# Performance work log

Measured on AMD Instinct MI355X. Metric: run time of the kernel, lower is better.

## Reference

```python
import jax, jax.numpy as jnp
import numpy as np

B, C, N, T = 32, 32, 300, 64      # batch, residual/conv channels, nodes, seq_len
DIM, K, SKIP, GD = 40, 20, 64, 2  # node_dim, top-k (subgraph_size), skip_channels, gcn_depth
TANH_A, PROP_A = 3.0, 0.05
KSET = (2, 3, 6, 7)
TOUT = T - (KSET[-1] - 1)          # 58: time length after dilated inception (dilation=1)


def conv2d(x, w, b):
    y = jax.lax.conv_general_dilated(x, w, (1, 1), 'VALID', dimension_numbers=('NCHW', 'OIHW', 'NCHW'))
    return y + b[None, :, None, None]


def setup_inputs() -> dict:
    key = jax.random.key(0)
    ks = iter(jax.random.split(key, 48))
    def nrm(shape, s=1.0):
        return jax.random.normal(next(ks), shape, jnp.float32) * s
    inp = {
        'x': nrm((B, C, N, T)),
        'x_skip': nrm((B, SKIP, N, 1)),
        'idx': jnp.arange(N, dtype=jnp.int32),
        'emb1': nrm((N, DIM), 0.1), 'emb2': nrm((N, DIM), 0.1),
        'lin1_w': nrm((DIM, DIM), 0.15), 'lin1_b': jnp.zeros((DIM,), jnp.float32),
        'lin2_w': nrm((DIM, DIM), 0.15), 'lin2_b': jnp.zeros((DIM,), jnp.float32),
        'skip_w': nrm((SKIP, C, 1, TOUT), 0.05), 'skip_b': jnp.zeros((SKIP,), jnp.float32),
        'mp1_w': nrm((C, (GD + 1) * C, 1, 1), 0.1), 'mp1_b': jnp.zeros((C,), jnp.float32),
        'mp2_w': nrm((C, (GD + 1) * C, 1, 1), 0.1), 'mp2_b': jnp.zeros((C,), jnp.float32),
        'ln_w': jnp.ones((C, N, TOUT), jnp.float32), 'ln_b': jnp.zeros((C, N, TOUT), jnp.float32),
    }
    for k in KSET:
        inp[f'fw{k}'] = nrm((C // 4, C, 1, k), 0.1); inp[f'fb{k}'] = jnp.zeros((C // 4,), jnp.float32)
        inp[f'gw{k}'] = nrm((C // 4, C, 1, k), 0.1); inp[f'gb{k}'] = jnp.zeros((C // 4,), jnp.float32)
    return inp


def _forward(x, x_skip, idx, emb1, emb2, lin1_w, lin1_b, lin2_w, lin2_b,
             fws, gws, skip_w, skip_b, mp1_w, mp1_b, mp2_w, mp2_b, ln_w, ln_b):
    # --- GraphConstructor: learned sparse adjacency via tanh/relu/top-k/scatter ---
    n1 = jnp.tanh(TANH_A * (emb1[idx] @ lin1_w.T + lin1_b))
    n2 = jnp.tanh(TANH_A * (emb2[idx] @ lin2_w.T + lin2_b))
    a = n1 @ n2.T - n2 @ n1.T
    A = jax.nn.relu(jnp.tanh(TANH_A * a))
    _, cols = jax.lax.top_k(A, K)                               # [N, K] per-row top-k indices
    mask = jnp.zeros_like(A).at[jnp.arange(N)[:, None], cols].set(1.0)
    A = A * mask
    # --- DilatedInception filter/gate (Conv2d kernel (1,k), crop to shortest) ---
    Xf = jnp.tanh(jnp.concatenate([conv2d(x, w, b)[..., -TOUT:] for w, b in fws], axis=1))
    Xg = jax.nn.sigmoid(jnp.concatenate([conv2d(x, w, b)[..., -TOUT:] for w, b in gws], axis=1))
    X = Xf * Xg                                                 # dropout is identity (training=False)
    X_skip_out = conv2d(X, skip_w, skip_b) + x_skip             # [B, SKIP, N, 1]
    # --- MixProp graph diffusion over A and A^T ---
    def mixprop(Xin, Adj, w, b):
        Ah = Adj + jnp.eye(N, dtype=Adj.dtype)
        Ah = Ah / Ah.sum(1)[:, None]                            # row-normalize
        H, hops = Xin, [Xin]
        for _ in range(GD):
            H = PROP_A * Xin + (1.0 - PROP_A) * jnp.einsum('bcwt,vw->bcvt', H, Ah)
            hops.append(H)
        return conv2d(jnp.concatenate(hops, axis=1), w, b)      # 1x1 conv: (GD+1)*C -> C
    X = mixprop(X, A, mp1_w, mp1_b) + mixprop(X, A.T, mp2_w, mp2_b)
    X = X + x[..., -TOUT:]
    # --- LayerNorm over (C, N, TOUT) with node-indexed affine ---
    mu = X.mean(axis=(1, 2, 3), keepdims=True)
    var = ((X - mu) ** 2).mean(axis=(1, 2, 3), keepdims=True)
    Xn = (X - mu) * jax.lax.rsqrt(var + 1e-5)
    X = Xn * ln_w[:, idx, :][None] + ln_b[:, idx, :][None]
    return X, X_skip_out


def reference(x, x_skip, idx, emb1, emb2, lin1_w, lin1_b, lin2_w, lin2_b,
              fw2, fb2, fw3, fb3, fw6, fb6, fw7, fb7,
              gw2, gb2, gw3, gb3, gw6, gb6, gw7, gb7,
              skip_w, skip_b, mp1_w, mp1_b, mp2_w, mp2_b, ln_w, ln_b):
    fws = [(fw2, fb2), (fw3, fb3), (fw6, fb6), (fw7, fb7)]
    gws = [(gw2, gb2), (gw3, gb3), (gw6, gb6), (gw7, gb7)]
    return _forward(x, x_skip, idx, emb1, emb2, lin1_w, lin1_b, lin2_w, lin2_b,
                    fws, gws, skip_w, skip_b, mp1_w, mp1_b, mp2_w, mp2_b, ln_w, ln_b)
```

## Files before the change

### kernel.cpp

```cpp
#include <hip/hip_runtime.h>
#include <hip/hip_bf16.h>
#include <math.h>

typedef __hip_bfloat16 bf16;
typedef __attribute__((ext_vector_type(8))) short bf16x8;
typedef __attribute__((ext_vector_type(4))) float f32x4;

#define NB 32
#define NC 32
#define NNODE 300
#define NT 64
#define NDIM 40
#define KTOP 20
#define NSKIP 64
#define NTOUT 58
#define SLAB 17400
#define BSLAB 556800
#define XEL 17817600
#define PSLAB 2048
#define BPSLAB 614400
#define XPEL 19660800

__device__ __forceinline__ float b2f(bf16 v){ return __bfloat162float(v); }
__device__ __forceinline__ bf16 f2b(float v){ return __float2bfloat16(v); }
__device__ __forceinline__ float fsig(float x){ return 1.0f/(1.0f + __expf(-x)); }
__device__ __forceinline__ float ftanh(float x){ return 2.0f*fsig(2.0f*x) - 1.0f; }

__device__ __forceinline__ unsigned short bbits(float v){
  bf16 h = f2b(v); unsigned short s; __builtin_memcpy(&s, &h, 2); return s;
}

__device__ __forceinline__ uint4 pack8(const float f[8]){
  uint4 d;
  d.x = (unsigned)bbits(f[0]) | ((unsigned)bbits(f[1]) << 16);
  d.y = (unsigned)bbits(f[2]) | ((unsigned)bbits(f[3]) << 16);
  d.z = (unsigned)bbits(f[4]) | ((unsigned)bbits(f[5]) << 16);
  d.w = (unsigned)bbits(f[6]) | ((unsigned)bbits(f[7]) << 16);
  return d;
}

__device__ __forceinline__ void bv_swz(int bid, int& b, int& v){
  int xcd = bid & 7, i = bid >> 3;
  int nb = xcd*1200 + i;
  b = nb / NNODE; v = nb - b*NNODE;
}

__global__ void k_nodes(const float* __restrict__ emb1, const float* __restrict__ emb2,
                        const float* __restrict__ l1w, const float* __restrict__ l1b,
                        const float* __restrict__ l2w, const float* __restrict__ l2b,
                        const int* __restrict__ idxp,
                        float* __restrict__ n1, float* __restrict__ n2){
  int i = blockIdx.x; int d = threadIdx.x;
  if (d >= NDIM) return;
  int r = idxp[i];
  float a1 = l1b[d], a2 = l2b[d];
  for (int k=0;k<NDIM;++k){
    a1 = fmaf(emb1[r*NDIM+k], l1w[d*NDIM+k], a1);
    a2 = fmaf(emb2[r*NDIM+k], l2w[d*NDIM+k], a2);
  }
  n1[i*NDIM+d] = tanhf(3.0f*a1);
  n2[i*NDIM+d] = tanhf(3.0f*a2);
}

__global__ void __launch_bounds__(64) k_adjrow(const float* __restrict__ n1,
                                               const float* __restrict__ n2,
                                               float* __restrict__ Am){
  int i = blockIdx.x; int lane = threadIdx.x;
  __shared__ float rowo[NNODE];
  __shared__ float rowv[NNODE];
  __shared__ int   sel[NNODE];
  for (int j=lane;j<NNODE;j+=64){
    float a = 0.f;
    #pragma unroll
    for (int k=0;k<NDIM;++k){
      float a1 = n1[i*NDIM+k], a2 = n2[i*NDIM+k];
      a = fmaf(a1, n2[j*NDIM+k], a);
      a = fmaf(-a2, n1[j*NDIM+k], a);
    }
    float v = tanhf(3.0f*a);
    v = v > 0.f ? v : 0.f;
    rowo[j]=v; rowv[j]=v; sel[j]=0;
  }
  __syncthreads();
  for (int it=0; it<KTOP; ++it){
    float best = -1.f; int bi = 0x7fffffff;
    for (int j=lane;j<NNODE;j+=64){
      float v = rowv[j];
      if (v > best){ best=v; bi=j; }
    }
    #pragma unroll
    for (int off=32; off; off>>=1){
      float ov = __shfl_xor(best, off);
      int   oi = __shfl_xor(bi, off);
      if (ov > best || (ov == best && oi < bi)){ best=ov; bi=oi; }
    }
    if (lane==0){ sel[bi]=1; rowv[bi]=-2.f; }
    __syncthreads();
  }
  for (int j=lane;j<NNODE;j+=64)
    Am[i*NNODE+j] = sel[j] ? rowo[j] : 0.f;
}

__global__ void __launch_bounds__(64) k_norm(const float* __restrict__ Am, float* __restrict__ Ah){
  int r = blockIdx.x;
  int side = r >= 304; int v = side ? r - 304 : r;
  float* dst = Ah + (size_t)(side ? 304*304 : 0) + v*304;
  int lane = threadIdx.x;
  if (v >= NNODE){
    for (int w=lane; w<304; w+=64) dst[w] = 0.f;
    return;
  }
  float s = 0.f;
  for (int w=lane; w<NNODE; w+=64)
    s += side ? Am[w*NNODE + v] : Am[v*NNODE + w];
  #pragma unroll
  for (int off=32; off; off>>=1) s += __shfl_xor(s, off);
  float inv = 1.0f/(s + 1.0f);
  for (int w=lane; w<304; w+=64){
    float a = (w < NNODE) ? (side ? Am[w*NNODE + v] : Am[v*NNODE + w]) : 0.f;
    if (w == v) a += 1.0f;
    dst[w] = a*inv;
  }
}

__global__ void k_mpk(const float* __restrict__ Ah, bf16* __restrict__ Mpk){
  int id = blockIdx.x*blockDim.x + threadIdx.x;
  if (id >= 4*320*320) return;
  int pm = id / (320*320);
  int rem = id % (320*320);
  int v = rem / 320, w = rem % 320;
  int s = pm >> 1, m = pm & 1;
  float val = 0.f;
  if (v < 304 && w < 304){
    const float* A = Ah + (size_t)s*304*304;
    float a = A[v*304 + w];
    if (m == 0){
      val = 0.95f*a + (v==w ? 0.05f : 0.f);
    } else {
      float d = 0.f;
      for (int u=0; u<304; ++u) d = fmaf(A[v*304 + u], A[u*304 + w], d);
      val = 0.9025f*d + 0.0475f*a + (v==w ? 0.05f : 0.f);
    }
  }
  int vt16 = v >> 4, lv = v & 15, ks = w >> 5, g = (w >> 3) & 3, j = w & 7;
  int lane = g*16 + lv;
  Mpk[(((size_t)(pm*20 + vt16)*10 + ks)*64 + lane)*8 + j] = f2b(val);
}

__global__ void k_wpack2(const float* __restrict__ fw2,const float* __restrict__ fw3,
                         const float* __restrict__ fw6,const float* __restrict__ fw7,
                         const float* __restrict__ gw2,const float* __restrict__ gw3,
                         const float* __restrict__ gw6,const float* __restrict__ gw7,
                         const float* __restrict__ fb2,const float* __restrict__ fb3,
                         const float* __restrict__ fb6,const float* __restrict__ fb7,
                         const float* __restrict__ gb2,const float* __restrict__ gb3,
                         const float* __restrict__ gb6,const float* __restrict__ gb7,
                         bf16* __restrict__ wfA, float* __restrict__ biasPk){
  int T = blockIdx.x*blockDim.x + threadIdx.x;
  if (T < 14336){
    int j = T & 7;
    int l = (T >> 3) & 63;
    int q = T >> 9;
    int d = q % 7, mt = q / 7;
    int m = mt*16 + (l & 15);
    int ic = (l >> 4)*8 + j;
    int c = m >> 1, path = m & 1;
    int cls = c >> 3, o = c & 7;
    int kk = (cls==0) ? 2 : (cls==1) ? 3 : (cls==2) ? 6 : 7;
    int tp = d - (7 - kk);
    float val = 0.f;
    if (tp >= 0){
      const float* w = (path==0)
        ? (cls==0?fw2:cls==1?fw3:cls==2?fw6:fw7)
        : (cls==0?gw2:cls==1?gw3:cls==2?gw6:gw7);
      val = w[(o*NC + ic)*kk + tp];
    }
    wfA[T] = f2b(val);
  } else if (T < 14336 + 32){
    int c = T - 14336;
    int cls = c >> 3, o = c & 7;
    const float* fb = cls==0?fb2:cls==1?fb3:cls==2?fb6:fb7;
    const float* gb = cls==0?gb2:cls==1?gb3:cls==2?gb6:gb7;
    biasPk[c*2]   = fb[o];
    biasPk[c*2+1] = gb[o];
  }
}

__global__ void k_wprepM(const float* __restrict__ m1w, const float* __restrict__ m2w,
                         const float* __restrict__ m1b, const float* __restrict__ m2b,
                         bf16* __restrict__ pkB0, bf16* __restrict__ pkB1,
                         float* __restrict__ biasSum){
  int id = blockIdx.x*blockDim.x + threadIdx.x;
  if (id < 3072){
    int j = id & 7, l = (id >> 3) & 63, q = id >> 9;
    int ks = q % 3, nt = q / 3;
    int k = (l >> 4)*8 + j;
    int c = nt*16 + (l & 15);
    float val;
    if      (ks == 0) val = m1w[c*96 + k] + m2w[c*96 + k];
    else if (ks == 1) val = m1w[c*96 + 32 + k];
    else              val = m1w[c*96 + 64 + k];
    pkB0[id] = f2b(val);
  } else if (id < 5120){
    int id2 = id - 3072;
    int j = id2 & 7, l = (id2 >> 3) & 63, q = id2 >> 9;
    int ks = q & 1, nt = q >> 1;
    int k = (l >> 4)*8 + j;
    int c = nt*16 + (l & 15);
    pkB1[id2] = f2b(ks==0 ? m2w[c*96 + 32 + k] : m2w[c*96 + 64 + k]);
  } else if (id < 5152){
    int c = id - 5120;
    biasSum[c] = m1b[c] + m2b[c];
  }
}

__global__ void k_wTb(const float* __restrict__ sw, bf16* __restrict__ wTb){
  int id = blockIdx.x*blockDim.x + threadIdx.x;
  if (id >= 131072) return;
  int j = id & 7, l = (id >> 3) & 63, q = id >> 9;
  int ks = q & 63, nt = q >> 6;
  int k = ks*32 + (l >> 4)*8 + j;
  int t = k >> 5, c = k & 31;
  int sc = nt*16 + (l & 15);
  float val = (t < NTOUT) ? sw[sc*1856 + c*NTOUT + t] : 0.f;
  wTb[id] = f2b(val);
}

__global__ void __launch_bounds__(256) k_incepM(const float* __restrict__ x,
    const bf16* __restrict__ wfA, const float* __restrict__ biasPk,
    bf16* __restrict__ Xp){
  __shared__ unsigned short xcm[72*32];
  int b, n; bv_swz(blockIdx.x, b, n);
  int bn = b*NNODE + n;
  int tid = threadIdx.x;
  {
    int c = tid >> 3, tq = tid & 7, t0 = tq*8;
    const float* src = x + ((size_t)(b*NC + c)*NNODE + n)*NT + t0;
    float4 v0 = *reinterpret_cast<const float4*>(src);
    float4 v1 = *reinterpret_cast<const float4*>(src + 4);
    float f[8] = {v0.x,v0.y,v0.z,v0.w,v1.x,v1.y,v1.z,v1.w};
    int gl = c >> 3, cl = c & 7;
    #pragma unroll
    for (int i=0;i<8;++i){
      int t = t0 + i;
      int pg = gl ^ ((t >> 3) & 3);
      xcm[t*32 + pg*8 + cl] = bbits(f[i]);
    }
    int zt = 64 + (tid >> 5), zic = tid & 31;
    int zpg = (zic >> 3) ^ ((zt >> 3) & 3);
    xcm[zt*32 + zpg*8 + (zic & 7)] = 0;
  }
  __syncthreads();
  int lane = tid & 63;
  int mt = __builtin_amdgcn_readfirstlane(tid >> 6);
  bf16x8 wA[7];
  #pragma unroll
  for (int d=0; d<7; ++d)
    wA[d] = *reinterpret_cast<const bf16x8*>(wfA + (size_t)((mt*7 + d)*64 + lane)*8);
  int g = lane >> 4, col = lane & 15;
  int c0 = mt*8 + 2*g;
  float4 bias2 = *reinterpret_cast<const float4*>(biasPk + c0*2);
  #pragma unroll
  for (int nt=0; nt<4; ++nt){
    int t = col + nt*16;
    f32x4 acc = {0.f, 0.f, 0.f, 0.f};
    #pragma unroll
    for (int d=0; d<7; ++d){
      int tr = t + d;
      int pg = g ^ ((tr >> 3) & 3);
      bf16x8 bfr = *reinterpret_cast<const bf16x8*>(&xcm[tr*32 + pg*8]);
      acc = __builtin_amdgcn_mfma_f32_16x16x32_bf16(wA[d], bfr, acc, 0, 0, 0);
    }
    bool act = t < NTOUT;
    float X0 = act ? (ftanh(acc[0] + bias2.x) * fsig(acc[1] + bias2.y)) : 0.f;
    float X1 = act ? (ftanh(acc[2] + bias2.z) * fsig(acc[3] + bias2.w)) : 0.f;
    unsigned pv = (unsigned)bbits(X0) | ((unsigned)bbits(X1) << 16);
    *reinterpret_cast<unsigned*>(Xp + (size_t)bn*PSLAB + t*32 + c0) = pv;
  }
}

__global__ void __launch_bounds__(256) k_xt(const bf16* __restrict__ Xp, bf16* __restrict__ XpT2){
  __shared__ unsigned short tile[64*66];
  int bid = blockIdx.x;
  int b = bid / 160, r = bid - b*160;
  int wt = r / 32, ctt2 = r - wt*32;
  int w0 = wt*64, ct0 = ctt2*64;
  int tid = threadIdx.x;
  #pragma unroll
  for (int p=0; p<2; ++p){
    int w_in = (tid >> 3) + p*32;
    int ct_in = (tid & 7)*8;
    int w = w0 + w_in;
    uint4 d = (w < NNODE)
      ? *reinterpret_cast<const uint4*>(Xp + (size_t)b*BPSLAB + (size_t)w*PSLAB + ct0 + ct_in)
      : make_uint4(0,0,0,0);
    unsigned short* t = tile + w_in*66 + ct_in;
    *reinterpret_cast<unsigned*>(t)     = d.x;
    *reinterpret_cast<unsigned*>(t + 2) = d.y;
    *reinterpret_cast<unsigned*>(t + 4) = d.z;
    *reinterpret_cast<unsigned*>(t + 6) = d.w;
  }
  __syncthreads();
  #pragma unroll
  for (int p=0; p<2; ++p){
    int ct_in = (tid >> 3) + p*32;
    int wq = tid & 7;
    unsigned short u[8];
    #pragma unroll
    for (int j=0;j<8;++j) u[j] = tile[(wq*8 + j)*66 + ct_in];
    uint4 d;
    d.x = (unsigned)u[0] | ((unsigned)u[1] << 16);
    d.y = (unsigned)u[2] | ((unsigned)u[3] << 16);
    d.z = (unsigned)u[4] | ((unsigned)u[5] << 16);
    d.w = (unsigned)u[6] | ((unsigned)u[7] << 16);
    int ct = ct0 + ct_in;
    int w = w0 + wq*8;
    int ks = w >> 5, w_in32 = w & 31;
    size_t addr = (((size_t)(b*16 + (ct >> 7))*10 + ks) << 12) + ((ct & 127) << 5) + w_in32;
    *reinterpret_cast<uint4*>(XpT2 + addr) = d;
  }
}

__global__ void __launch_bounds__(256) k_skipM(const bf16* __restrict__ Xp, const bf16* __restrict__ wTb,
      const float* __restrict__ skip_b, const float* __restrict__ x_skip, float* __restrict__ out){
  int bn0 = blockIdx.x * 16;
  int tid = threadIdx.x, lane = tid & 63;
  int nt = __builtin_amdgcn_readfirstlane(tid >> 6);
  int g = lane >> 4, col = lane & 15;
  const bf16* aptr = Xp + (size_t)(bn0 + col)*PSLAB + g*8;
  const bf16* bptr = wTb + ((size_t)nt*64*64 + lane)*8;
  f32x4 acc = {0.f, 0.f, 0.f, 0.f};
  #pragma unroll 4
  for (int ks=0; ks<64; ++ks){
    bf16x8 aF = *reinterpret_cast<const bf16x8*>(aptr + ks*32);
    bf16x8 bF = *reinterpret_cast<const bf16x8*>(bptr + (size_t)ks*512);
    acc = __builtin_amdgcn_mfma_f32_16x16x32_bf16(aF, bF, acc, 0, 0, 0);
  }
  int sc = nt*16 + col;
  float sb = skip_b[sc];
  #pragma unroll
  for (int r=0;r<4;++r){
    int bn = bn0 + g*4 + r;
    int b = bn / NNODE, n = bn - b*NNODE;
    size_t so = (size_t)b*NSKIP*NNODE + (size_t)sc*NNODE + n;
    out[(size_t)XEL + so] = acc[r] + sb + x_skip[so];
  }
}

__global__ void __launch_bounds__(256) k_hop(const bf16* __restrict__ XpT2,
    const bf16* __restrict__ Mpk, bf16* __restrict__ H1, bf16* __restrict__ H2, int pass){
  __shared__ unsigned short bst[128*72];
  __shared__ __align__(16) unsigned short outT[64*136];
  int bid = blockIdx.x;
  int xcd = bid & 7, i = bid >> 3;
  int nb = xcd*640 + i;
  int b = nb / 160; int r = nb - b*160;
  int m = r / 80; r -= m*80;
  int vt = r >> 4; int ctt = r & 15;
  int ct0 = ctt*128, v0 = vt*64;
  int tid = threadIdx.x, lane = tid & 63;
  int mt = __builtin_amdgcn_readfirstlane(tid >> 6);
  int g = lane >> 4, col = lane & 15;
  const bf16* mbase = Mpk + (((size_t)((pass*2 + m)*20 + vt*4 + mt)*10)*64 + lane)*8;
  bf16x8 aF[10];
  #pragma unroll
  for (int ks=0; ks<10; ++ks)
    aF[ks] = *reinterpret_cast<const bf16x8*>(mbase + (size_t)ks*512);
  const bf16* tb = XpT2 + (((size_t)(b*16 + ctt)*10) << 12);
  int s_ct = tid >> 2, s_w = (tid & 3)*8;
  f32x4 acc[8];
  #pragma unroll
  for (int nt=0; nt<8; ++nt) acc[nt] = (f32x4){0.f,0.f,0.f,0.f};
  for (int ks=0; ks<10; ++ks){
    __syncthreads();
    const bf16* src = tb + ((size_t)ks << 12);
    {
      uint4 d0 = *reinterpret_cast<const uint4*>(src + s_ct*32 + s_w);
      uint4 d1 = *reinterpret_cast<const uint4*>(src + (s_ct+64)*32 + s_w);
      *reinterpret_cast<uint4*>(bst + s_ct*72 + s_w)      = d0;
      *reinterpret_cast<uint4*>(bst + (s_ct+64)*72 + s_w) = d1;
    }
    __syncthreads();
    #pragma unroll
    for (int nt=0; nt<8; ++nt){
      bf16x8 bF = *reinterpret_cast<const bf16x8*>(bst + (nt*16 + col)*72 + g*8);
      acc[nt] = __builtin_amdgcn_mfma_f32_16x16x32_bf16(aF[ks], bF, acc[nt], 0, 0, 0);
    }
  }
  #pragma unroll
  for (int nt=0; nt<8; ++nt){
    #pragma unroll
    for (int r4=0; r4<4; ++r4)
      outT[(mt*16 + g*4 + r4)*136 + nt*16 + col] = bbits(acc[nt][r4]);
  }
  __syncthreads();
  bf16* Hout = (m == 0) ? H1 : H2;
  {
    int vl = tid >> 2, e = tid & 3;
    int v = v0 + vl;
    if (v < NNODE){
      bf16* dst = Hout + (size_t)b*BPSLAB + (size_t)v*PSLAB + ct0;
      #pragma unroll
      for (int h=0; h<4; ++h){
        int ctl = e*32 + h*8;
        uint4 d = *reinterpret_cast<const uint4*>(outT + vl*136 + ctl);
        *reinterpret_cast<uint4*>(dst + ctl) = d;
      }
    }
  }
}

__global__ void __launch_bounds__(256) k_fuse0(bf16* __restrict__ Xp,
    const bf16* __restrict__ H1, const bf16* __restrict__ H2,
    const bf16* __restrict__ pkB, const float* __restrict__ biasSum){
  int b, v; bv_swz(blockIdx.x, b, v);
  size_t vbase = (size_t)b*BPSLAB + (size_t)v*PSLAB;
  int tid = threadIdx.x, lane = tid & 63;
  int mt = __builtin_amdgcn_readfirstlane(tid >> 6);
  int g = lane >> 4, col = lane & 15;
  int tRow = mt*16 + col;
  bf16x8 aX = *reinterpret_cast<const bf16x8*>(Xp + vbase + tRow*32 + g*8);
  bf16x8 a1 = *reinterpret_cast<const bf16x8*>(H1 + vbase + tRow*32 + g*8);
  bf16x8 a2 = *reinterpret_cast<const bf16x8*>(H2 + vbase + tRow*32 + g*8);
  __syncthreads();
  int t0 = mt*16 + g*4;
  bf16* pp = Xp + vbase;
  #pragma unroll
  for (int nt=0; nt<2; ++nt){
    int c_out = nt*16 + col;
    float bv = biasSum[c_out];
    f32x4 acc = {bv, bv, bv, bv};
    bf16x8 w0 = *reinterpret_cast<const bf16x8*>(pkB + (size_t)((nt*3+0)*64 + lane)*8);
    bf16x8 w1 = *reinterpret_cast<const bf16x8*>(pkB + (size_t)((nt*3+1)*64 + lane)*8);
    bf16x8 w2 = *reinterpret_cast<const bf16x8*>(pkB + (size_t)((nt*3+2)*64 + lane)*8);
    acc = __builtin_amdgcn_mfma_f32_16x16x32_bf16(aX, w0, acc, 0, 0, 0);
    acc = __builtin_amdgcn_mfma_f32_16x16x32_bf16(a1, w1, acc, 0, 0, 0);
    acc = __builtin_amdgcn_mfma_f32_16x16x32_bf16(a2, w2, acc, 0, 0, 0);
    #pragma unroll
    for (int r=0;r<4;++r)
      pp[(t0 + r)*32 + c_out] = f2b(acc[r]);
  }
}

__global__ void __launch_bounds__(256) k_fuse1(const bf16* __restrict__ P,
    const bf16* __restrict__ H1, const bf16* __restrict__ H2,
    float* __restrict__ out, const float* __restrict__ x,
    const bf16* __restrict__ pkB, double* __restrict__ part2){
  __shared__ float redS[4], redS2[4];
  int b, v; bv_swz(blockIdx.x, b, v);
  size_t vbase = (size_t)b*BPSLAB + (size_t)v*PSLAB;
  int tid = threadIdx.x, lane = tid & 63;
  int mt = __builtin_amdgcn_readfirstlane(tid >> 6);
  int g = lane >> 4, col = lane & 15;
  int tRow = mt*16 + col;
  bf16x8 a1 = *reinterpret_cast<const bf16x8*>(H1 + vbase + tRow*32 + g*8);
  bf16x8 a2 = *reinterpret_cast<const bf16x8*>(H2 + vbase + tRow*32 + g*8);
  int t0 = mt*16 + g*4;
  const bf16* pp = P + vbase;
  float s = 0.f, s2 = 0.f;
  #pragma unroll
  for (int nt=0; nt<2; ++nt){
    int c_out = nt*16 + col;
    f32x4 acc = {0.f, 0.f, 0.f, 0.f};
    bf16x8 w0 = *reinterpret_cast<const bf16x8*>(pkB + (size_t)((nt*2+0)*64 + lane)*8);
    bf16x8 w1 = *reinterpret_cast<const bf16x8*>(pkB + (size_t)((nt*2+1)*64 + lane)*8);
    acc = __builtin_amdgcn_mfma_f32_16x16x32_bf16(a1, w0, acc, 0, 0, 0);
    acc = __builtin_amdgcn_mfma_f32_16x16x32_bf16(a2, w1, acc, 0, 0, 0);
    float* po = out + ((size_t)(b*NC + c_out)*NNODE + v)*NTOUT + t0;
    const float* rx = x + ((size_t)(b*NC + c_out)*NNODE + v)*NT + 6 + t0;
    if (t0 <= 54){
      float2 r0 = *reinterpret_cast<const float2*>(rx);
      float2 r1 = *reinterpret_cast<const float2*>(rx + 2);
      float f0 = b2f(pp[(t0+0)*32 + c_out]) + acc[0] + r0.x;
      float f1 = b2f(pp[(t0+1)*32 + c_out]) + acc[1] + r0.y;
      float f2v = b2f(pp[(t0+2)*32 + c_out]) + acc[2] + r1.x;
      float f3 = b2f(pp[(t0+3)*32 + c_out]) + acc[3] + r1.y;
      *reinterpret_cast<float2*>(po)     = make_float2(f0, f1);
      *reinterpret_cast<float2*>(po + 2) = make_float2(f2v, f3);
      s  += f0 + f1 + f2v + f3;
      s2 += f0*f0 + f1*f1 + f2v*f2v + f3*f3;
    } else if (t0 == 56){
      float2 r0 = *reinterpret_cast<const float2*>(rx);
      float f0 = b2f(pp[(t0+0)*32 + c_out]) + acc[0] + r0.x;
      float f1 = b2f(pp[(t0+1)*32 + c_out]) + acc[1] + r0.y;
      *reinterpret_cast<float2*>(po) = make_float2(f0, f1);
      s  += f0 + f1;
      s2 += f0*f0 + f1*f1;
    }
  }
  #pragma unroll
  for (int o=32; o; o>>=1){ s += __shfl_down(s, o); s2 += __shfl_down(s2, o); }
  if (lane == 0){ redS[mt] = s; redS2[mt] = s2; }
  __syncthreads();
  if (tid == 0){
    float as = redS[0]+redS[1]+redS[2]+redS[3];
    float as2 = redS2[0]+redS2[1]+redS2[2]+redS2[3];
    atomicAdd(&part2[b*2],   (double)as);
    atomicAdd(&part2[b*2+1], (double)as2);
  }
}

__global__ void k_lnfin(const double* __restrict__ part2, float* __restrict__ stats){
  int b = threadIdx.x; if (b >= 32) return;
  double s = part2[b*2], s2 = part2[b*2+1];
  double n = (double)BSLAB;
  double mean = s/n;
  double var = s2/n - mean*mean;
  stats[b*2]   = (float)mean;
  stats[b*2+1] = (float)(1.0/sqrt(var + 1e-5));
}

__global__ void __launch_bounds__(256) k_lnapply(float* __restrict__ out, const float* __restrict__ stats,
        const float* __restrict__ lnw, const float* __restrict__ lnb, const int* __restrict__ idxp){
  int o = blockIdx.x*256 + threadIdx.x;
  int t = o % NTOUT; int v = (o / NTOUT) % NNODE; int c = (o / SLAB) % NC; int b = o / BSLAB;
  float mean = stats[b*2], rstd = stats[b*2+1];
  int vn = idxp[v];
  float wv = lnw[((size_t)c*NNODE + vn)*NTOUT + t];
  float bv = lnb[((size_t)c*NNODE + vn)*NTOUT + t];
  float vx = out[o];
  out[o] = (vx - mean)*rstd*wv + bv;
}

extern "C" void kernel_launch(void* const* d_in, const int* in_sizes, int n_in,
                              void* d_out, int out_size, void* d_ws, size_t ws_size,
                              hipStream_t stream) {
  (void)in_sizes; (void)n_in; (void)out_size; (void)ws_size;
  const float* x     = (const float*)d_in[0];
  const float* xskip = (const float*)d_in[1];
  const int*   idxp  = (const int*)d_in[2];
  const float* emb1  = (const float*)d_in[3];
  const float* emb2  = (const float*)d_in[4];
  const float* l1w   = (const float*)d_in[5];
  const float* l1b   = (const float*)d_in[6];
  const float* l2w   = (const float*)d_in[7];
  const float* l2b   = (const float*)d_in[8];
  const float* skw   = (const float*)d_in[9];
  const float* skb   = (const float*)d_in[10];
  const float* m1w   = (const float*)d_in[11];
  const float* m1b   = (const float*)d_in[12];
  const float* m2w   = (const float*)d_in[13];
  const float* m2b   = (const float*)d_in[14];
  const float* lnw   = (const float*)d_in[15];
  const float* lnb   = (const float*)d_in[16];
  const float* fw2=(const float*)d_in[17]; const float* fb2=(const float*)d_in[18];
  const float* gw2=(const float*)d_in[19]; const float* gb2=(const float*)d_in[20];
  const float* fw3=(const float*)d_in[21]; const float* fb3=(const float*)d_in[22];
  const float* gw3=(const float*)d_in[23]; const float* gb3=(const float*)d_in[24];
  const float* fw6=(const float*)d_in[25]; const float* fb6=(const float*)d_in[26];
  const float* gw6=(const float*)d_in[27]; const float* gb6=(const float*)d_in[28];
  const float* fw7=(const float*)d_in[29]; const float* fb7=(const float*)d_in[30];
  const float* gw7=(const float*)d_in[31]; const float* gb7=(const float*)d_in[32];
  float* out = (float*)d_out;

  char* wsbase = (char*)d_ws;
  size_t cur = 0;
  auto alloc = [&](size_t bytes)->char*{
    char* p = wsbase + cur;
    cur = (cur + bytes + 255) & ~(size_t)255;
    return p;
  };
  bf16*  Xp   = (bf16*) alloc((size_t)XPEL*2);
  bf16*  H1   = (bf16*) alloc((size_t)XPEL*2);
  bf16*  H2   = (bf16*) alloc((size_t)XPEL*2);
  bf16*  XpT2 = (bf16*) alloc((size_t)NB*16*10*4096*2);
  float* n1   = (float*)alloc(12000*4);
  float* n2   = (float*)alloc(12000*4);
  float* Am   = (float*)alloc(90000*4);
  float* Ah   = (float*)alloc(2*304*304*4);
  bf16*  Mpk  = (bf16*) alloc((size_t)4*20*10*64*8*2);
  bf16*  wTb  = (bf16*) alloc(131072*2);
  bf16*  wfA  = (bf16*) alloc(14336*2);
  float* biasPk = (float*)alloc(64*4);
  bf16*  pkB0 = (bf16*) alloc(3072*2);
  bf16*  pkB1 = (bf16*) alloc(2048*2);
  float* biasSum = (float*)alloc(32*4);
  double* part2 = (double*)alloc(64*8);
  float* stats = (float*)alloc(64*4);

  hipMemsetAsync(part2, 0, 64*sizeof(double), stream);

  k_nodes <<<NNODE, 64, 0, stream>>>(emb1, emb2, l1w, l1b, l2w, l2b, idxp, n1, n2);
  k_adjrow<<<NNODE, 64, 0, stream>>>(n1, n2, Am);
  k_norm  <<<608, 64, 0, stream>>>(Am, Ah);
  k_mpk   <<<1600, 256, 0, stream>>>(Ah, Mpk);

  k_wpack2<<<57, 256, 0, stream>>>(fw2,fw3,fw6,fw7, gw2,gw3,gw6,gw7,
                                   fb2,fb3,fb6,fb7, gb2,gb3,gb6,gb7, wfA, biasPk);
  k_wprepM<<<21, 256, 0, stream>>>(m1w, m2w, m1b, m2b, pkB0, pkB1, biasSum);
  k_wTb   <<<512, 256, 0, stream>>>(skw, wTb);

  k_incepM<<<NB*NNODE, 256, 0, stream>>>(x, wfA, biasPk, Xp);

  k_xt<<<5120, 256, 0, stream>>>(Xp, XpT2);

  k_skipM<<<(NB*NNODE)/16, 256, 0, stream>>>(Xp, wTb, skb, xskip, out);

  k_hop  <<<5120, 256, 0, stream>>>(XpT2, Mpk, H1, H2, 0);
  k_fuse0<<<NB*NNODE, 256, 0, stream>>>(Xp, H1, H2, pkB0, biasSum);

  k_hop  <<<5120, 256, 0, stream>>>(XpT2, Mpk, H1, H2, 1);
  k_fuse1<<<NB*NNODE, 256, 0, stream>>>(Xp, H1, H2, out, x, pkB1, part2);

  k_lnfin<<<1, 32, 0, stream>>>(part2, stats);
  k_lnapply<<<XEL/256, 256, 0, stream>>>(out, stats, lnw, lnb, idxp);
}
```

Before: 419.9 us.

## Merge both hop passes into one launch and fuse mixprop projections

Runs both propagation passes (A and A^T powers) in a single hop launch, with the pass index taken from the block id, and writes into four separate H buffers. A single fused kernel then applies all five weight blocks (X, H1a, H2a, H1b, H2b) in one MFMA chain. This removes the intermediate write and re-read of Xp between passes and cuts two kernel launches. The cost is two extra full-size bf16 buffers of workspace and more loads per block in the fuse kernel.

```diff
diff --git a/kernel.cpp b/kernel.cpp
--- a/kernel.cpp
+++ b/kernel.cpp
@@ -188,26 +188,20 @@
 
 __global__ void k_wprepM(const float* __restrict__ m1w, const float* __restrict__ m2w,
                          const float* __restrict__ m1b, const float* __restrict__ m2b,
-                         bf16* __restrict__ pkB0, bf16* __restrict__ pkB1,
-                         float* __restrict__ biasSum){
+                         bf16* __restrict__ pkB, float* __restrict__ biasSum){
   int id = blockIdx.x*blockDim.x + threadIdx.x;
-  if (id < 3072){
+  if (id < 5120){
     int j = id & 7, l = (id >> 3) & 63, q = id >> 9;
-    int ks = q % 3, nt = q / 3;
+    int ks = q % 5, nt = q / 5;
     int k = (l >> 4)*8 + j;
     int c = nt*16 + (l & 15);
     float val;
     if      (ks == 0) val = m1w[c*96 + k] + m2w[c*96 + k];
     else if (ks == 1) val = m1w[c*96 + 32 + k];
-    else              val = m1w[c*96 + 64 + k];
-    pkB0[id] = f2b(val);
-  } else if (id < 5120){
-    int id2 = id - 3072;
-    int j = id2 & 7, l = (id2 >> 3) & 63, q = id2 >> 9;
-    int ks = q & 1, nt = q >> 1;
-    int k = (l >> 4)*8 + j;
-    int c = nt*16 + (l & 15);
-    pkB1[id2] = f2b(ks==0 ? m2w[c*96 + 32 + k] : m2w[c*96 + 64 + k]);
+    else if (ks == 2) val = m1w[c*96 + 64 + k];
+    else if (ks == 3) val = m2w[c*96 + 32 + k];
+    else              val = m2w[c*96 + 64 + k];
+    pkB[id] = f2b(val);
   } else if (id < 5152){
     int c = id - 5120;
     biasSum[c] = m1b[c] + m2b[c];
@@ -348,11 +342,16 @@
 }
 
 __global__ void __launch_bounds__(256) k_hop(const bf16* __restrict__ XpT2,
-    const bf16* __restrict__ Mpk, bf16* __restrict__ H1, bf16* __restrict__ H2, int pass){
+    const bf16* __restrict__ Mpk,
+    bf16* __restrict__ H1a, bf16* __restrict__ H2a,
+    bf16* __restrict__ H1b, bf16* __restrict__ H2b){
   __shared__ unsigned short bst[128*72];
   __shared__ __align__(16) unsigned short outT[64*136];
   int bid = blockIdx.x;
-  int xcd = bid & 7, i = bid >> 3;
+  int xcd = bid & 7;
+  int q = bid >> 3;
+  int pass = q & 1;
+  int i = q >> 1;
   int nb = xcd*640 + i;
   int b = nb / 160; int r = nb - b*160;
   int m = r / 80; r -= m*80;
@@ -394,7 +393,7 @@
       outT[(mt*16 + g*4 + r4)*136 + nt*16 + col] = bbits(acc[nt][r4]);
   }
   __syncthreads();
-  bf16* Hout = (m == 0) ? H1 : H2;
+  bf16* Hout = pass == 0 ? (m == 0 ? H1a : H2a) : (m == 0 ? H1b : H2b);
   {
     int vl = tid >> 2, e = tid & 3;
     int v = v0 + vl;
@@ -410,42 +409,12 @@
   }
 }
 
-__global__ void __launch_bounds__(256) k_fuse0(bf16* __restrict__ Xp,
-    const bf16* __restrict__ H1, const bf16* __restrict__ H2,
-    const bf16* __restrict__ pkB, const float* __restrict__ biasSum){
-  int b, v; bv_swz(blockIdx.x, b, v);
-  size_t vbase = (size_t)b*BPSLAB + (size_t)v*PSLAB;
-  int tid = threadIdx.x, lane = tid & 63;
-  int mt = __builtin_amdgcn_readfirstlane(tid >> 6);
-  int g = lane >> 4, col = lane & 15;
-  int tRow = mt*16 + col;
-  bf16x8 aX = *reinterpret_cast<const bf16x8*>(Xp + vbase + tRow*32 + g*8);
-  bf16x8 a1 = *reinterpret_cast<const bf16x8*>(H1 + vbase + tRow*32 + g*8);
-  bf16x8 a2 = *reinterpret_cast<const bf16x8*>(H2 + vbase + tRow*32 + g*8);
-  __syncthreads();
-  int t0 = mt*16 + g*4;
-  bf16* pp = Xp + vbase;
-  #pragma unroll
-  for (int nt=0; nt<2; ++nt){
-    int c_out = nt*16 + col;
-    float bv = biasSum[c_out];
-    f32x4 acc = {bv, bv, bv, bv};
-    bf16x8 w0 = *reinterpret_cast<const bf16x8*>(pkB + (size_t)((nt*3+0)*64 + lane)*8);
-    bf16x8 w1 = *reinterpret_cast<const bf16x8*>(pkB + (size_t)((nt*3+1)*64 + lane)*8);
-    bf16x8 w2 = *reinterpret_cast<const bf16x8*>(pkB + (size_t)((nt*3+2)*64 + lane)*8);
-    acc = __builtin_amdgcn_mfma_f32_16x16x32_bf16(aX, w0, acc, 0, 0, 0);
-    acc = __builtin_amdgcn_mfma_f32_16x16x32_bf16(a1, w1, acc, 0, 0, 0);
-    acc = __builtin_amdgcn_mfma_f32_16x16x32_bf16(a2, w2, acc, 0, 0, 0);
-    #pragma unroll
-    for (int r=0;r<4;++r)
-      pp[(t0 + r)*32 + c_out] = f2b(acc[r]);
-  }
-}
-
-__global__ void __launch_bounds__(256) k_fuse1(const bf16* __restrict__ P,
-    const bf16* __restrict__ H1, const bf16* __restrict__ H2,
+__global__ void __launch_bounds__(256) k_fuseM(const bf16* __restrict__ Xp,
+    const bf16* __restrict__ H1a, const bf16* __restrict__ H2a,
+    const bf16* __restrict__ H1b, const bf16* __restrict__ H2b,
     float* __restrict__ out, const float* __restrict__ x,
-    const bf16* __restrict__ pkB, double* __restrict__ part2){
+    const bf16* __restrict__ pkB, const float* __restrict__ biasSum,
+    double* __restrict__ part2){
   __shared__ float redS[4], redS2[4];
   int b, v; bv_swz(blockIdx.x, b, v);
   size_t vbase = (size_t)b*BPSLAB + (size_t)v*PSLAB;
@@ -453,36 +422,43 @@
   int mt = __builtin_amdgcn_readfirstlane(tid >> 6);
   int g = lane >> 4, col = lane & 15;
   int tRow = mt*16 + col;
-  bf16x8 a1 = *reinterpret_cast<const bf16x8*>(H1 + vbase + tRow*32 + g*8);
-  bf16x8 a2 = *reinterpret_cast<const bf16x8*>(H2 + vbase + tRow*32 + g*8);
+  size_t fo = vbase + tRow*32 + g*8;
+  bf16x8 aX  = *reinterpret_cast<const bf16x8*>(Xp  + fo);
+  bf16x8 a1a = *reinterpret_cast<const bf16x8*>(H1a + fo);
+  bf16x8 a2a = *reinterpret_cast<const bf16x8*>(H2a + fo);
+  bf16x8 a1b = *reinterpret_cast<const bf16x8*>(H1b + fo);
+  bf16x8 a2b = *reinterpret_cast<const bf16x8*>(H2b + fo);
   int t0 = mt*16 + g*4;
-  const bf16* pp = P + vbase;
   float s = 0.f, s2 = 0.f;
   #pragma unroll
   for (int nt=0; nt<2; ++nt){
     int c_out = nt*16 + col;
-    f32x4 acc = {0.f, 0.f, 0.f, 0.f};
-    bf16x8 w0 = *reinterpret_cast<const bf16x8*>(pkB + (size_t)((nt*2+0)*64 + lane)*8);
-    bf16x8 w1 = *reinterpret_cast<const bf16x8*>(pkB + (size_t)((nt*2+1)*64 + lane)*8);
-    acc = __builtin_amdgcn_mfma_f32_16x16x32_bf16(a1, w0, acc, 0, 0, 0);
-    acc = __builtin_amdgcn_mfma_f32_16x16x32_bf16(a2, w1, acc, 0, 0, 0);
+    float bv = biasSum[c_out];
+    f32x4 acc = {bv, bv, bv, bv};
+    bf16x8 w0 = *reinterpret_cast<const bf16x8*>(pkB + (size_t)((nt*5+0)*64 + lane)*8);
+    bf16x8 w1 = *reinterpret_cast<const bf16x8*>(pkB + (size_t)((nt*5+1)*64 + lane)*8);
+    bf16x8 w2 = *reinterpret_cast<const bf16x8*>(pkB + (size_t)((nt*5+2)*64 + lane)*8);
+    bf16x8 w3 = *reinterpret_cast<const bf16x8*>(pkB + (size_t)((nt*5+3)*64 + lane)*8);
+    bf16x8 w4 = *reinterpret_cast<const bf16x8*>(pkB + (size_t)((nt*5+4)*64 + lane)*8);
+    acc = __builtin_amdgcn_mfma_f32_16x16x32_bf16(aX,  w0, acc, 0, 0, 0);
+    acc = __builtin_amdgcn_mfma_f32_16x16x32_bf16(a1a, w1, acc, 0, 0, 0);
+    acc = __builtin_amdgcn_mfma_f32_16x16x32_bf16(a2a, w2, acc, 0, 0, 0);
+    acc = __builtin_amdgcn_mfma_f32_16x16x32_bf16(a1b, w3, acc, 0, 0, 0);
+    acc = __builtin_amdgcn_mfma_f32_16x16x32_bf16(a2b, w4, acc, 0, 0, 0);
     float* po = out + ((size_t)(b*NC + c_out)*NNODE + v)*NTOUT + t0;
     const float* rx = x + ((size_t)(b*NC + c_out)*NNODE + v)*NT + 6 + t0;
     if (t0 <= 54){
       float2 r0 = *reinterpret_cast<const float2*>(rx);
       float2 r1 = *reinterpret_cast<const float2*>(rx + 2);
-      float f0 = b2f(pp[(t0+0)*32 + c_out]) + acc[0] + r0.x;
-      float f1 = b2f(pp[(t0+1)*32 + c_out]) + acc[1] + r0.y;
-      float f2v = b2f(pp[(t0+2)*32 + c_out]) + acc[2] + r1.x;
-      float f3 = b2f(pp[(t0+3)*32 + c_out]) + acc[3] + r1.y;
+      float f0 = acc[0] + r0.x, f1 = acc[1] + r0.y;
+      float f2v = acc[2] + r1.x, f3 = acc[3] + r1.y;
       *reinterpret_cast<float2*>(po)     = make_float2(f0, f1);
       *reinterpret_cast<float2*>(po + 2) = make_float2(f2v, f3);
       s  += f0 + f1 + f2v + f3;
       s2 += f0*f0 + f1*f1 + f2v*f2v + f3*f3;
     } else if (t0 == 56){
       float2 r0 = *reinterpret_cast<const float2*>(rx);
-      float f0 = b2f(pp[(t0+0)*32 + c_out]) + acc[0] + r0.x;
-      float f1 = b2f(pp[(t0+1)*32 + c_out]) + acc[1] + r0.y;
+      float f0 = acc[0] + r0.x, f1 = acc[1] + r0.y;
       *reinterpret_cast<float2*>(po) = make_float2(f0, f1);
       s  += f0 + f1;
       s2 += f0*f0 + f1*f1;
@@ -561,8 +537,10 @@
     return p;
   };
   bf16*  Xp   = (bf16*) alloc((size_t)XPEL*2);
-  bf16*  H1   = (bf16*) alloc((size_t)XPEL*2);
-  bf16*  H2   = (bf16*) alloc((size_t)XPEL*2);
+  bf16*  H1a  = (bf16*) alloc((size_t)XPEL*2);
+  bf16*  H2a  = (bf16*) alloc((size_t)XPEL*2);
+  bf16*  H1b  = (bf16*) alloc((size_t)XPEL*2);
+  bf16*  H2b  = (bf16*) alloc((size_t)XPEL*2);
   bf16*  XpT2 = (bf16*) alloc((size_t)NB*16*10*4096*2);
   float* n1   = (float*)alloc(12000*4);
   float* n2   = (float*)alloc(12000*4);
@@ -572,8 +550,7 @@
   bf16*  wTb  = (bf16*) alloc(131072*2);
   bf16*  wfA  = (bf16*) alloc(14336*2);
   float* biasPk = (float*)alloc(64*4);
-  bf16*  pkB0 = (bf16*) alloc(3072*2);
-  bf16*  pkB1 = (bf16*) alloc(2048*2);
+  bf16*  pkB  = (bf16*) alloc(5120*2);
   float* biasSum = (float*)alloc(32*4);
   double* part2 = (double*)alloc(64*8);
   float* stats = (float*)alloc(64*4);
@@ -587,7 +564,7 @@
 
   k_wpack2<<<57, 256, 0, stream>>>(fw2,fw3,fw6,fw7, gw2,gw3,gw6,gw7,
                                    fb2,fb3,fb6,fb7, gb2,gb3,gb6,gb7, wfA, biasPk);
-  k_wprepM<<<21, 256, 0, stream>>>(m1w, m2w, m1b, m2b, pkB0, pkB1, biasSum);
+  k_wprepM<<<21, 256, 0, stream>>>(m1w, m2w, m1b, m2b, pkB, biasSum);
   k_wTb   <<<512, 256, 0, stream>>>(skw, wTb);
 
   k_incepM<<<NB*NNODE, 256, 0, stream>>>(x, wfA, biasPk, Xp);
@@ -596,11 +573,9 @@
 
   k_skipM<<<(NB*NNODE)/16, 256, 0, stream>>>(Xp, wTb, skb, xskip, out);
 
-  k_hop  <<<5120, 256, 0, stream>>>(XpT2, Mpk, H1, H2, 0);
-  k_fuse0<<<NB*NNODE, 256, 0, stream>>>(Xp, H1, H2, pkB0, biasSum);
-
-  k_hop  <<<5120, 256, 0, stream>>>(XpT2, Mpk, H1, H2, 1);
-  k_fuse1<<<NB*NNODE, 256, 0, stream>>>(Xp, H1, H2, out, x, pkB1, part2);
+  k_hop<<<10240, 256, 0, stream>>>(XpT2, Mpk, H1a, H2a, H1b, H2b);
+
+  k_fuseM<<<NB*NNODE, 256, 0, stream>>>(Xp, H1a, H2a, H1b, H2b, out, x, pkB, biasSum, part2);
 
   k_lnfin<<<1, 32, 0, stream>>>(part2, stats);
   k_lnapply<<<XEL/256, 256, 0, stream>>>(out, stats, lnw, lnb, idxp);
```

Measured after the change: 412.5 us. No clear change (-1.8%).
